# Kernel optimization log

Hardware: AMD Instinct MI355X
Metric: run time of the kernel (lower is better)

## Reference

```python
import jax, jax.numpy as jnp
import numpy as np

N_NODES = 100000
EMB_DIM = 128
HIDDEN = 128
N_EDGES = 1600000
N_LABEL = 200000


def _xavier(key, shape):
    fan_in, fan_out = shape[1], shape[0]
    lim = float(np.sqrt(6.0 / (fan_in + fan_out)))
    return jax.random.uniform(key, shape, jnp.float32, -lim, lim)


def setup_inputs() -> dict:
    key = jax.random.key(0)
    ks = jax.random.split(key, 8)
    n_id = jnp.arange(N_NODES, dtype=jnp.int64) if jax.config.jax_enable_x64 else jnp.arange(N_NODES, dtype=jnp.int32)
    edge_index = jax.random.randint(ks[0], (2, N_EDGES), 0, N_NODES)
    edge_label_index = jax.random.randint(ks[1], (2, N_LABEL), 0, N_NODES)
    emb_weight = _xavier(ks[2], (N_NODES, EMB_DIM))
    # layer 0: in=EMB_DIM -> HIDDEN ; layer 1: HIDDEN -> HIDDEN
    Wl0 = _xavier(ks[3], (HIDDEN, EMB_DIM))
    bl0 = jnp.zeros((HIDDEN,), jnp.float32)
    Wr0 = _xavier(ks[4], (HIDDEN, EMB_DIM))
    Wl1 = _xavier(ks[5], (HIDDEN, HIDDEN))
    bl1 = jnp.zeros((HIDDEN,), jnp.float32)
    Wr1 = _xavier(ks[6], (HIDDEN, HIDDEN))
    return {
        "n_id": n_id,
        "edge_index": edge_index,
        "edge_label_index": edge_label_index,
        "emb_weight": emb_weight,
        "Wl0": Wl0, "bl0": bl0, "Wr0": Wr0,
        "Wl1": Wl1, "bl1": bl1, "Wr1": Wr1,
    }


def _sage_conv(x, src, dst, Wl, bl, Wr, num_nodes):
    # PyG SAGEConv (aggr='mean'): out = lin_l(mean_{j in N(i)} x_j) + lin_r(x_i)
    agg = jax.ops.segment_sum(x[src], dst, num_segments=num_nodes)  # [N, D]
    deg = jax.ops.segment_sum(jnp.ones((src.shape[0],), x.dtype), dst, num_segments=num_nodes)
    mean = agg / jnp.maximum(deg, 1.0)[:, None]
    return mean @ Wl.T + bl + x @ Wr.T


def reference(n_id, edge_index, edge_label_index, emb_weight, Wl0, bl0, Wr0, Wl1, bl1, Wr1):
    src, dst = edge_index[0], edge_index[1]
    num_nodes = n_id.shape[0]
    x = emb_weight[n_id]                                  # [N, EMB_DIM]
    x = _sage_conv(x, src, dst, Wl0, bl0, Wr0, num_nodes)  # layer 0
    x = jax.nn.relu(x)                                     # relu between layers (dropout p=0, eval)
    z = _sage_conv(x, src, dst, Wl1, bl1, Wr1, num_nodes)  # layer 1 (no relu after last)
    s, d = edge_label_index[0], edge_label_index[1]
    return jnp.sum(z[s] * z[d], axis=-1)                   # [N_LABEL]
```

## Files before the change

### kernel.cpp

```cpp
#include <hip/hip_runtime.h>
#include <hip/hip_bf16.h>

typedef short bf16x8 __attribute__((ext_vector_type(8)));
typedef float f32x4 __attribute__((ext_vector_type(4)));
typedef float f32x2 __attribute__((ext_vector_type(2)));

#define BKT_SHIFT 9
#define BKT_RANGE 512
#define MAXBKT 256

__device__ __forceinline__ float bf2f(unsigned short u){
  union { unsigned int i; float f; } v; v.i = ((unsigned int)u)<<16; return v.f;
}
__device__ __forceinline__ unsigned short f2bf(float f){
  union { float f; unsigned int i; } v; v.f = f;
  unsigned int i = v.i;
  return (unsigned short)((i + 0x7fffu + ((i>>16)&1u)) >> 16);
}
__device__ __forceinline__ f32x2 up2(unsigned int v){
  union { unsigned int i; float f; } lo, hi;
  lo.i = v << 16; hi.i = v & 0xffff0000u;
  return (f32x2){lo.f, hi.f};
}

__global__ void k_bcount(const int* dst, int* gcount, int ne, int nbk){
  __shared__ int cnt[MAXBKT];
  int tid = threadIdx.x;
  if(tid < nbk) cnt[tid] = 0;
  __syncthreads();
  int base = blockIdx.x * 4096;
#pragma unroll
  for(int i=0;i<16;++i){
    int e = base + i*256 + tid;
    if(e < ne) atomicAdd(&cnt[dst[e] >> BKT_SHIFT], 1);
  }
  __syncthreads();
  if(tid < nbk && cnt[tid] > 0) atomicAdd(&gcount[tid], cnt[tid]);
}

__global__ void k_bscatter_prep(const int* src, const int* dst, const int* gcount,
                                int* gcur0, unsigned int* ebuf, int ne, int nbk, int nch,
                                const float* emb, const int* n_id, unsigned short* A0,
                                const float* Wl0, const float* Wr0, unsigned short* wc0,
                                const float* Wl1, const float* Wr1, unsigned short* wc1,
                                int n){
  int b = blockIdx.x;
  int tid = threadIdx.x;
  if(b >= nch){
    int pb = b - nch;
    if(pb < 256){
      const float* Wl = (pb < 128) ? Wl0 : Wl1;
      const float* Wr = (pb < 128) ? Wr0 : Wr1;
      unsigned short* wc = (pb < 128) ? wc0 : wc1;
      int i = (pb & 127)*256 + tid;
      int nn = i >> 8, k = i & 255;
      float v = (k<128) ? Wl[nn*128 + k] : Wr[nn*128 + k - 128];
      wc[i] = f2bf(v);
    } else {
      int gid = (pb-256)*256 + tid;
      int row = gid >> 5, c4 = (gid & 31) * 4;
      if(row >= n) return;
      float4 v = *(const float4*)&emb[(long)n_id[row]*128 + c4];
      ushort4 o;
      o.x = f2bf(v.x); o.y = f2bf(v.y); o.z = f2bf(v.z); o.w = f2bf(v.w);
      *(ushort4*)&A0[(long)row*256 + 128 + c4] = o;
    }
    return;
  }
  __shared__ int cnt[MAXBKT];
  __shared__ int runbase[MAXBKT];
  __shared__ int sg[MAXBKT];
  cnt[tid] = 0;
  sg[tid] = (tid < nbk) ? gcount[tid] : 0;
  __syncthreads();
  int base = b * 4096;
  int pk[16], bk[16], re[16];
#pragma unroll
  for(int i=0;i<16;++i){
    int e = base + i*256 + tid;
    if(e < ne){
      int d = dst[e];
      bk[i] = d >> BKT_SHIFT;
      pk[i] = (unsigned)src[e] | ((unsigned)(d & (BKT_RANGE-1)) << 17);
      re[i] = atomicAdd(&cnt[bk[i]], 1);
    } else bk[i] = -1;
  }
  int myv = sg[tid];
  __syncthreads();
  for(int off=1; off<256; off<<=1){
    int a = (tid>=off) ? sg[tid-off] : 0;
    __syncthreads();
    sg[tid] += a;
    __syncthreads();
  }
  if(tid < nbk)
    runbase[tid] = (sg[tid] - myv) + (cnt[tid] ? atomicAdd(&gcur0[tid], cnt[tid]) : 0);
  __syncthreads();
#pragma unroll
  for(int i=0;i<16;++i){
    if(bk[i] >= 0) ebuf[runbase[bk[i]] + re[i]] = pk[i];
  }
}

__global__ void k_bsort(const unsigned int* ebuf, const int* gcount,
                        int* csr, int* row_off, int n, int ne, int nbk){
  __shared__ int sg[MAXBKT];
  __shared__ int h[BKT_RANGE];
  __shared__ int cur[BKT_RANGE];
  __shared__ int sm[512];
  int t = threadIdx.x;
  int k = blockIdx.x;
  if(t < MAXBKT) sg[t] = (t < nbk) ? gcount[t] : 0;
  __syncthreads();
  for(int off=1; off<256; off<<=1){
    int a = (t>=off && t<256) ? sg[t-off] : 0;
    __syncthreads();
    if(t<256) sg[t] += a;
    __syncthreads();
  }
  int beg = sg[k] - gcount[k];
  int end = sg[k];
  int lo = k << BKT_SHIFT;
  h[t] = 0;
  __syncthreads();
  for(int e = beg + t; e < end; e += 512)
    atomicAdd(&h[ebuf[e] >> 17], 1);
  __syncthreads();
  int v = h[t];
  sm[t] = v;
  __syncthreads();
  for(int off=1; off<512; off<<=1){
    int a = (t>=off) ? sm[t-off] : 0;
    __syncthreads();
    sm[t] += a;
    __syncthreads();
  }
  int excl = beg + sm[t] - v;
  cur[t] = excl;
  if(lo + t < n) row_off[lo + t] = excl;
  if(k == nbk-1 && t == 0) row_off[n] = ne;
  __syncthreads();
  for(int e = beg + t; e < end; e += 512){
    unsigned int p = ebuf[e];
    int pos = atomicAdd(&cur[p >> 17], 1);
    csr[pos] = (int)(p & 0x1FFFFu);
  }
}

__global__ void k_agg(const unsigned short* X, unsigned short* Mout,
                      const int* row_off, const int* csr, int n){
  int w = __builtin_amdgcn_readfirstlane((int)((blockIdx.x*blockDim.x + threadIdx.x) >> 6));
  int lane = threadIdx.x & 63;
  if(w >= n) return;
  int beg = row_off[w], end = row_off[w+1];
  int deg = end - beg;
  f32x2 acc = {0.f, 0.f};
  const char* Xb = (const char*)X + 256;
  int e = beg;
  for(; e + 8 <= end; e += 8){
    unsigned int v0 = ((const unsigned int*)(Xb + (long)csr[e  ]*512))[lane];
    unsigned int v1 = ((const unsigned int*)(Xb + (long)csr[e+1]*512))[lane];
    unsigned int v2 = ((const unsigned int*)(Xb + (long)csr[e+2]*512))[lane];
    unsigned int v3 = ((const unsigned int*)(Xb + (long)csr[e+3]*512))[lane];
    unsigned int v4 = ((const unsigned int*)(Xb + (long)csr[e+4]*512))[lane];
    unsigned int v5 = ((const unsigned int*)(Xb + (long)csr[e+5]*512))[lane];
    unsigned int v6 = ((const unsigned int*)(Xb + (long)csr[e+6]*512))[lane];
    unsigned int v7 = ((const unsigned int*)(Xb + (long)csr[e+7]*512))[lane];
    acc += up2(v0); acc += up2(v1); acc += up2(v2); acc += up2(v3);
    acc += up2(v4); acc += up2(v5); acc += up2(v6); acc += up2(v7);
  }
  for(; e + 4 <= end; e += 4){
    unsigned int v0 = ((const unsigned int*)(Xb + (long)csr[e  ]*512))[lane];
    unsigned int v1 = ((const unsigned int*)(Xb + (long)csr[e+1]*512))[lane];
    unsigned int v2 = ((const unsigned int*)(Xb + (long)csr[e+2]*512))[lane];
    unsigned int v3 = ((const unsigned int*)(Xb + (long)csr[e+3]*512))[lane];
    acc += up2(v0); acc += up2(v1); acc += up2(v2); acc += up2(v3);
  }
  for(; e < end; ++e){
    unsigned int v = ((const unsigned int*)(Xb + (long)csr[e]*512))[lane];
    acc += up2(v);
  }
  float inv = (deg>0) ? 1.0f/(float)deg : 0.f;
  float a0 = acc[0]*inv, a1 = acc[1]*inv;
  unsigned int o = ((unsigned int)f2bf(a1) << 16) | (unsigned int)f2bf(a0);
  *(unsigned int*)((char*)Mout + (long)w*512 + lane*4) = o;
}

template<int RELU, int OUTSTRIDE, int OUTOFF>
__global__ __launch_bounds__(256,2) void k_gemm(const unsigned short* A,
                                                const unsigned short* wc,
                                                const float* bias,
                                                unsigned short* out, int nrows){
  __shared__ unsigned short Wl[32768];
  int tid = threadIdx.x;
  for(int it=0; it<16; ++it){
    int idx  = it*256 + tid;
    int byte = idx*16;
    int row  = byte >> 9;
    int swz  = byte ^ ((row & 7) << 4);
    *(uint4*)((char*)Wl + swz) = *(const uint4*)((const char*)wc + byte);
  }
  __syncthreads();

  int lane = tid & 63, wv = tid >> 6;
  float bs[8];
#pragma unroll
  for(int nf=0; nf<8; ++nf) bs[nf] = bias[nf*16 + (lane & 15)];

  for(int t=0; t<4; ++t){
    int rowA = blockIdx.x*256 + t*64 + wv*16 + (lane & 15);
    int rcl  = rowA < nrows ? rowA : nrows-1;
    const char* Ab = (const char*)(A + (long)rcl*256) + ((lane>>4)*16);
    bf16x8 a[8];
#pragma unroll
    for(int k=0;k<8;++k) a[k] = *(const bf16x8*)(Ab + k*64);

    f32x4 acc[8];
#pragma unroll
    for(int i=0;i<8;++i) acc[i] = (f32x4){0.f,0.f,0.f,0.f};

#pragma unroll
    for(int nf=0; nf<8; ++nf){
      int rw = nf*16 + (lane & 15);
#pragma unroll
      for(int k=0;k<8;++k){
        int byte = (rw*512 + k*64 + (lane>>4)*16) ^ ((rw & 7) << 4);
        bf16x8 b = *(const bf16x8*)((const char*)Wl + byte);
        acc[nf] = __builtin_amdgcn_mfma_f32_16x16x32_bf16(a[k], b, acc[nf], 0, 0, 0);
      }
    }

    int rbase = blockIdx.x*256 + t*64 + wv*16 + (lane>>4)*4;
#pragma unroll
    for(int nf=0; nf<8; ++nf){
      int col = nf*16 + (lane & 15);
#pragma unroll
      for(int r=0;r<4;++r){
        int row = rbase + r;
        if(row < nrows){
          float v = acc[nf][r] + bs[nf];
          if(RELU) v = v > 0.f ? v : 0.f;
          out[(long)row*OUTSTRIDE + OUTOFF + col] = f2bf(v);
        }
      }
    }
  }
}

__global__ void k_dot(const unsigned short* z, const int* s, const int* d,
                      float* out, int nl){
  int wv = (blockIdx.x*256 + threadIdx.x) >> 6;
  int lane = threadIdx.x & 63;
  int g = lane >> 4;
  int gl = lane & 15;
  int pi = wv*4 + g;
  float acc = 0.f;
  if(pi < nl){
    int si = s[pi], di = d[pi];
    bf16x8 va = *(const bf16x8*)&z[(long)si*128 + gl*8];
    bf16x8 vb = *(const bf16x8*)&z[(long)di*128 + gl*8];
#pragma unroll
    for(int i=0;i<8;++i)
      acc += bf2f((unsigned short)va[i]) * bf2f((unsigned short)vb[i]);
#pragma unroll
    for(int off=1; off<16; off<<=1)
      acc += __shfl_xor(acc, off, 16);
    if(gl==0) out[pi] = acc;
  }
}

extern "C" void kernel_launch(void* const* d_in, const int* in_sizes, int n_in,
                              void* d_out, int out_size, void* d_ws, size_t ws_size,
                              hipStream_t stream){
  const int N  = in_sizes[0];
  const int NE = in_sizes[1] / 2;
  const int NL = in_sizes[2] / 2;
  const int*   n_id = (const int*)d_in[0];
  const int*   src  = (const int*)d_in[1];
  const int*   dst  = src + NE;
  const int*   ls   = (const int*)d_in[2];
  const int*   ld   = ls + NL;
  const float* emb  = (const float*)d_in[3];
  const float* Wl0  = (const float*)d_in[4];
  const float* bl0  = (const float*)d_in[5];
  const float* Wr0  = (const float*)d_in[6];
  const float* Wl1  = (const float*)d_in[7];
  const float* bl1  = (const float*)d_in[8];
  const float* Wr1  = (const float*)d_in[9];
  float* out = (float*)d_out;

  char* ws = (char*)d_ws;
  size_t off = 0;
  auto alloc = [&](size_t bytes)->char*{
    char* p = ws + off;
    off = (off + bytes + 255) & ~(size_t)255;
    return p;
  };
  unsigned short* A0   = (unsigned short*)alloc((size_t)N*256*2);
  unsigned short* A1   = (unsigned short*)alloc((size_t)N*256*2);
  int* row_off         = (int*)alloc((size_t)(N+1)*4);
  int* csr             = (int*)alloc((size_t)NE*4);
  int* gcount          = (int*)alloc(MAXBKT*4*2);
  int* gcur0           = gcount + MAXBKT;
  unsigned short* wc0  = (unsigned short*)alloc(128*256*2);
  unsigned short* wc1  = (unsigned short*)alloc(128*256*2);
  unsigned int* ebuf   = (unsigned int*)A1;
  unsigned short* Z    = A0;

  const int NBK = (N + BKT_RANGE - 1) >> BKT_SHIFT;
  const int NCH = (NE + 4095) / 4096;

  hipMemsetAsync(gcount, 0, MAXBKT*4*2, stream);
  hipLaunchKernelGGL(k_bcount, dim3(NCH), dim3(256), 0, stream, dst, gcount, NE, NBK);
  hipLaunchKernelGGL(k_bscatter_prep, dim3(NCH + 256 + (N*32+255)/256), dim3(256), 0, stream,
                     src, dst, gcount, gcur0, ebuf, NE, NBK, NCH,
                     emb, n_id, A0, Wl0, Wr0, wc0, Wl1, Wr1, wc1, N);
  hipLaunchKernelGGL(k_bsort, dim3(NBK), dim3(512), 0, stream,
                     ebuf, gcount, csr, row_off, N, NE, NBK);
  hipLaunchKernelGGL(k_agg, dim3((N*64+255)/256), dim3(256), 0, stream, A0, A0, row_off, csr, N);
  hipLaunchKernelGGL((k_gemm<1,256,128>), dim3((N+255)/256), dim3(256), 0, stream, A0, wc0, bl0, A1, N);
  hipLaunchKernelGGL(k_agg, dim3((N*64+255)/256), dim3(256), 0, stream, A1, A1, row_off, csr, N);
  hipLaunchKernelGGL((k_gemm<0,128,0>), dim3((N+255)/256), dim3(256), 0, stream, A1, wc1, bl1, Z, N);
  hipLaunchKernelGGL(k_dot, dim3((NL+15)/16), dim3(256), 0, stream, Z, ls, ld, out, NL);
}
```

Baseline: 260.2 us.

## Fuse CSR bucket sort with layer-0 mean aggregation using smaller buckets

Buckets shrink from 512 to 128 destination nodes, and the bucket prefix scan moves into a separate single-block kernel, so the scatter and sort kernels no longer redo it per block. The per-bucket sort kernel now also performs the first layer's mean aggregation. It reads source indices from a shared-memory copy of the sorted bucket (with a global fallback when a bucket exceeds capacity), which removes one kernel launch and the CSR re-read. The cost is 782 blocks of 512 threads each doing only 128 nodes, so each wave handles 16 nodes serially, which may lower parallelism compared with the separate one-wave-per-node aggregation kernel.

```diff
diff --git a/kernel.cpp b/kernel.cpp
--- a/kernel.cpp
+++ b/kernel.cpp
@@ -5,9 +5,10 @@
 typedef float f32x4 __attribute__((ext_vector_type(4)));
 typedef float f32x2 __attribute__((ext_vector_type(2)));
 
-#define BKT_SHIFT 9
-#define BKT_RANGE 512
-#define MAXBKT 256
+#define BKT_SHIFT 7
+#define BKT_RANGE 128
+#define MAXBKT 1024
+#define CAP 4096
 
 __device__ __forceinline__ float bf2f(unsigned short u){
   union { unsigned int i; float f; } v; v.i = ((unsigned int)u)<<16; return v.f;
@@ -26,7 +27,7 @@
 __global__ void k_bcount(const int* dst, int* gcount, int ne, int nbk){
   __shared__ int cnt[MAXBKT];
   int tid = threadIdx.x;
-  if(tid < nbk) cnt[tid] = 0;
+  for(int i=tid; i<MAXBKT; i+=256) cnt[i] = 0;
   __syncthreads();
   int base = blockIdx.x * 4096;
 #pragma unroll
@@ -35,10 +36,26 @@
     if(e < ne) atomicAdd(&cnt[dst[e] >> BKT_SHIFT], 1);
   }
   __syncthreads();
-  if(tid < nbk && cnt[tid] > 0) atomicAdd(&gcount[tid], cnt[tid]);
-}
-
-__global__ void k_bscatter_prep(const int* src, const int* dst, const int* gcount,
+  for(int i=tid; i<nbk; i+=256) if(cnt[i]) atomicAdd(&gcount[i], cnt[i]);
+}
+
+__global__ void k_bscan(const int* gcount, int* gbase, int nbk, int ne){
+  __shared__ int sm[MAXBKT];
+  int t = threadIdx.x;
+  int v = (t<nbk) ? gcount[t] : 0;
+  sm[t] = v;
+  __syncthreads();
+  for(int off=1; off<MAXBKT; off<<=1){
+    int a = (t>=off) ? sm[t-off] : 0;
+    __syncthreads();
+    sm[t] += a;
+    __syncthreads();
+  }
+  if(t<nbk) gbase[t] = sm[t] - v;
+  if(t==nbk-1) gbase[nbk] = sm[t];
+}
+
+__global__ void k_bscatter_prep(const int* src, const int* dst, const int* gbase,
                                 int* gcur0, unsigned int* ebuf, int ne, int nbk, int nch,
                                 const float* emb, const int* n_id, unsigned short* A0,
                                 const float* Wl0, const float* Wr0, unsigned short* wc0,
@@ -69,9 +86,7 @@
   }
   __shared__ int cnt[MAXBKT];
   __shared__ int runbase[MAXBKT];
-  __shared__ int sg[MAXBKT];
-  cnt[tid] = 0;
-  sg[tid] = (tid < nbk) ? gcount[tid] : 0;
+  for(int i=tid; i<MAXBKT; i+=256) cnt[i] = 0;
   __syncthreads();
   int base = b * 4096;
   int pk[16], bk[16], re[16];
@@ -85,16 +100,9 @@
       re[i] = atomicAdd(&cnt[bk[i]], 1);
     } else bk[i] = -1;
   }
-  int myv = sg[tid];
-  __syncthreads();
-  for(int off=1; off<256; off<<=1){
-    int a = (tid>=off) ? sg[tid-off] : 0;
-    __syncthreads();
-    sg[tid] += a;
-    __syncthreads();
-  }
-  if(tid < nbk)
-    runbase[tid] = (sg[tid] - myv) + (cnt[tid] ? atomicAdd(&gcur0[tid], cnt[tid]) : 0);
+  __syncthreads();
+  for(int i=tid; i<nbk; i+=256)
+    runbase[i] = gbase[i] + (cnt[i] ? atomicAdd(&gcur0[i], cnt[i]) : 0);
   __syncthreads();
 #pragma unroll
   for(int i=0;i<16;++i){
@@ -102,48 +110,104 @@
   }
 }
 
-__global__ void k_bsort(const unsigned int* ebuf, const int* gcount,
-                        int* csr, int* row_off, int n, int ne, int nbk){
-  __shared__ int sg[MAXBKT];
+__global__ __launch_bounds__(512) void k_aggsort(const unsigned int* ebuf, const int* gbase,
+                                                 const unsigned short* X, unsigned short* Mout,
+                                                 int* csr, int* row_off, int n, int ne, int nbk){
   __shared__ int h[BKT_RANGE];
+  __shared__ int ends[BKT_RANGE];
   __shared__ int cur[BKT_RANGE];
-  __shared__ int sm[512];
-  int t = threadIdx.x;
-  int k = blockIdx.x;
-  if(t < MAXBKT) sg[t] = (t < nbk) ? gcount[t] : 0;
-  __syncthreads();
-  for(int off=1; off<256; off<<=1){
-    int a = (t>=off && t<256) ? sg[t-off] : 0;
+  __shared__ int eb[CAP];
+  int t = threadIdx.x, k = blockIdx.x;
+  int beg = gbase[k], end = gbase[k+1];
+  int cnt = end - beg;
+  bool lok = (cnt <= CAP);
+  if(t < BKT_RANGE) h[t] = 0;
+  __syncthreads();
+  for(int e=t; e<cnt; e+=512) atomicAdd(&h[ebuf[beg+e] >> 17], 1);
+  __syncthreads();
+  int v0 = (t < BKT_RANGE) ? h[t] : 0;
+  for(int off=1; off<BKT_RANGE; off<<=1){
+    int a = (t>=off && t<BKT_RANGE) ? h[t-off] : 0;
     __syncthreads();
-    if(t<256) sg[t] += a;
+    if(t<BKT_RANGE) h[t] += a;
     __syncthreads();
   }
-  int beg = sg[k] - gcount[k];
-  int end = sg[k];
-  int lo = k << BKT_SHIFT;
-  h[t] = 0;
-  __syncthreads();
-  for(int e = beg + t; e < end; e += 512)
-    atomicAdd(&h[ebuf[e] >> 17], 1);
-  __syncthreads();
-  int v = h[t];
-  sm[t] = v;
-  __syncthreads();
-  for(int off=1; off<512; off<<=1){
-    int a = (t>=off) ? sm[t-off] : 0;
-    __syncthreads();
-    sm[t] += a;
-    __syncthreads();
-  }
-  int excl = beg + sm[t] - v;
-  cur[t] = excl;
-  if(lo + t < n) row_off[lo + t] = excl;
-  if(k == nbk-1 && t == 0) row_off[n] = ne;
-  __syncthreads();
-  for(int e = beg + t; e < end; e += 512){
-    unsigned int p = ebuf[e];
+  if(t < BKT_RANGE){
+    ends[t] = h[t];
+    cur[t]  = h[t] - v0;
+    int node = (k<<BKT_SHIFT) + t;
+    if(node < n) row_off[node] = beg + h[t] - v0;
+  }
+  if(k==nbk-1 && t==0) row_off[n] = ne;
+  __syncthreads();
+  for(int e=t; e<cnt; e+=512){
+    unsigned int p = ebuf[beg+e];
     int pos = atomicAdd(&cur[p >> 17], 1);
-    csr[pos] = (int)(p & 0x1FFFFu);
+    int s = (int)(p & 0x1FFFFu);
+    if(lok) eb[pos] = s;
+    csr[beg + pos] = s;
+  }
+  __syncthreads();
+  int wv = t >> 6, lane = t & 63;
+  const char* Xb = (const char*)X + 256;
+  const int* gsrc = csr + beg;
+  for(int i = wv*16; i < wv*16+16; ++i){
+    int node = (k<<BKT_SHIFT) + i;
+    if(node >= n) continue;
+    int lbeg = i ? ends[i-1] : 0;
+    int lend = ends[i];
+    int deg = lend - lbeg;
+    f32x2 acc = {0.f, 0.f};
+    if(lok){
+      int e = lbeg;
+      for(; e+8 <= lend; e += 8){
+        int s0=eb[e],s1=eb[e+1],s2=eb[e+2],s3=eb[e+3],s4=eb[e+4],s5=eb[e+5],s6=eb[e+6],s7=eb[e+7];
+        unsigned int v0 = ((const unsigned int*)(Xb + (long)s0*512))[lane];
+        unsigned int v1 = ((const unsigned int*)(Xb + (long)s1*512))[lane];
+        unsigned int v2 = ((const unsigned int*)(Xb + (long)s2*512))[lane];
+        unsigned int v3 = ((const unsigned int*)(Xb + (long)s3*512))[lane];
+        unsigned int v4 = ((const unsigned int*)(Xb + (long)s4*512))[lane];
+        unsigned int v5 = ((const unsigned int*)(Xb + (long)s5*512))[lane];
+        unsigned int v6 = ((const unsigned int*)(Xb + (long)s6*512))[lane];
+        unsigned int v7 = ((const unsigned int*)(Xb + (long)s7*512))[lane];
+        acc += up2(v0); acc += up2(v1); acc += up2(v2); acc += up2(v3);
+        acc += up2(v4); acc += up2(v5); acc += up2(v6); acc += up2(v7);
+      }
+      for(; e+4 <= lend; e += 4){
+        int s0=eb[e],s1=eb[e+1],s2=eb[e+2],s3=eb[e+3];
+        unsigned int v0 = ((const unsigned int*)(Xb + (long)s0*512))[lane];
+        unsigned int v1 = ((const unsigned int*)(Xb + (long)s1*512))[lane];
+        unsigned int v2 = ((const unsigned int*)(Xb + (long)s2*512))[lane];
+        unsigned int v3 = ((const unsigned int*)(Xb + (long)s3*512))[lane];
+        acc += up2(v0); acc += up2(v1); acc += up2(v2); acc += up2(v3);
+      }
+      for(; e < lend; ++e){
+        unsigned int v = ((const unsigned int*)(Xb + (long)eb[e]*512))[lane];
+        acc += up2(v);
+      }
+    } else {
+      int e = lbeg;
+      for(; e+8 <= lend; e += 8){
+        int s0=gsrc[e],s1=gsrc[e+1],s2=gsrc[e+2],s3=gsrc[e+3],s4=gsrc[e+4],s5=gsrc[e+5],s6=gsrc[e+6],s7=gsrc[e+7];
+        unsigned int v0 = ((const unsigned int*)(Xb + (long)s0*512))[lane];
+        unsigned int v1 = ((const unsigned int*)(Xb + (long)s1*512))[lane];
+        unsigned int v2 = ((const unsigned int*)(Xb + (long)s2*512))[lane];
+        unsigned int v3 = ((const unsigned int*)(Xb + (long)s3*512))[lane];
+        unsigned int v4 = ((const unsigned int*)(Xb + (long)s4*512))[lane];
+        unsigned int v5 = ((const unsigned int*)(Xb + (long)s5*512))[lane];
+        unsigned int v6 = ((const unsigned int*)(Xb + (long)s6*512))[lane];
+        unsigned int v7 = ((const unsigned int*)(Xb + (long)s7*512))[lane];
+        acc += up2(v0); acc += up2(v1); acc += up2(v2); acc += up2(v3);
+        acc += up2(v4); acc += up2(v5); acc += up2(v6); acc += up2(v7);
+      }
+      for(; e < lend; ++e){
+        unsigned int v = ((const unsigned int*)(Xb + (long)gsrc[e]*512))[lane];
+        acc += up2(v);
+      }
+    }
+    float inv = (deg>0) ? 1.0f/(float)deg : 0.f;
+    unsigned int o = ((unsigned int)f2bf(acc[1]*inv) << 16) | (unsigned int)f2bf(acc[0]*inv);
+    *(unsigned int*)((char*)Mout + (long)node*512 + lane*4) = o;
   }
 }
 
@@ -300,8 +364,9 @@
   unsigned short* A1   = (unsigned short*)alloc((size_t)N*256*2);
   int* row_off         = (int*)alloc((size_t)(N+1)*4);
   int* csr             = (int*)alloc((size_t)NE*4);
-  int* gcount          = (int*)alloc(MAXBKT*4*2);
+  int* gcount          = (int*)alloc(MAXBKT*4*3 + 4);
   int* gcur0           = gcount + MAXBKT;
+  int* gbase           = gcount + MAXBKT*2;
   unsigned short* wc0  = (unsigned short*)alloc(128*256*2);
   unsigned short* wc1  = (unsigned short*)alloc(128*256*2);
   unsigned int* ebuf   = (unsigned int*)A1;
@@ -312,12 +377,12 @@
 
   hipMemsetAsync(gcount, 0, MAXBKT*4*2, stream);
   hipLaunchKernelGGL(k_bcount, dim3(NCH), dim3(256), 0, stream, dst, gcount, NE, NBK);
+  hipLaunchKernelGGL(k_bscan, dim3(1), dim3(MAXBKT), 0, stream, gcount, gbase, NBK, NE);
   hipLaunchKernelGGL(k_bscatter_prep, dim3(NCH + 256 + (N*32+255)/256), dim3(256), 0, stream,
-                     src, dst, gcount, gcur0, ebuf, NE, NBK, NCH,
+                     src, dst, gbase, gcur0, ebuf, NE, NBK, NCH,
                      emb, n_id, A0, Wl0, Wr0, wc0, Wl1, Wr1, wc1, N);
-  hipLaunchKernelGGL(k_bsort, dim3(NBK), dim3(512), 0, stream,
-                     ebuf, gcount, csr, row_off, N, NE, NBK);
-  hipLaunchKernelGGL(k_agg, dim3((N*64+255)/256), dim3(256), 0, stream, A0, A0, row_off, csr, N);
+  hipLaunchKernelGGL(k_aggsort, dim3(NBK), dim3(512), 0, stream,
+                     ebuf, gbase, A0, A0, csr, row_off, N, NE, NBK);
   hipLaunchKernelGGL((k_gemm<1,256,128>), dim3((N+255)/256), dim3(256), 0, stream, A0, wc0, bl0, A1, N);
   hipLaunchKernelGGL(k_agg, dim3((N*64+255)/256), dim3(256), 0, stream, A1, A1, row_off, csr, N);
   hipLaunchKernelGGL((k_gemm<0,128,0>), dim3((N+255)/256), dim3(256), 0, stream, A1, wc1, bl1, Z, N);
```

Result: slower. 267.1 us (+2.6%).

## Split aggregation into feature slices with edge-parallel lanes and wave reduction

Applied to the files above, without the earlier changes.

Restructures the mean-aggregation kernel so each block handles one 32-byte feature slice (of 8) for a run of nodes. Lanes within a wave are spread across 8 edges at a time instead of 64 lanes covering one full row, and a shuffle reduction combines the partial sums. The aim is to raise memory-level parallelism and to make concurrently running blocks that share a slice reuse the same L2 lines. Loads and stores are marked nontemporal. The cost is much less bytes per gather (32B segments), plus extra shuffle and masking work; low-degree nodes waste lanes.

```diff
diff --git a/kernel.cpp b/kernel.cpp
--- a/kernel.cpp
+++ b/kernel.cpp
@@ -8,6 +8,7 @@
 #define BKT_SHIFT 9
 #define BKT_RANGE 512
 #define MAXBKT 256
+#define NPW 8
 
 __device__ __forceinline__ float bf2f(unsigned short u){
   union { unsigned int i; float f; } v; v.i = ((unsigned int)u)<<16; return v.f;
@@ -149,41 +150,48 @@
 
 __global__ void k_agg(const unsigned short* X, unsigned short* Mout,
                       const int* row_off, const int* csr, int n){
-  int w = __builtin_amdgcn_readfirstlane((int)((blockIdx.x*blockDim.x + threadIdx.x) >> 6));
+  int s = blockIdx.x & 7;
+  int chunk = blockIdx.x >> 3;
+  int wv = threadIdx.x >> 6;
   int lane = threadIdx.x & 63;
-  if(w >= n) return;
-  int beg = row_off[w], end = row_off[w+1];
-  int deg = end - beg;
-  f32x2 acc = {0.f, 0.f};
-  const char* Xb = (const char*)X + 256;
-  int e = beg;
-  for(; e + 8 <= end; e += 8){
-    unsigned int v0 = ((const unsigned int*)(Xb + (long)csr[e  ]*512))[lane];
-    unsigned int v1 = ((const unsigned int*)(Xb + (long)csr[e+1]*512))[lane];
-    unsigned int v2 = ((const unsigned int*)(Xb + (long)csr[e+2]*512))[lane];
-    unsigned int v3 = ((const unsigned int*)(Xb + (long)csr[e+3]*512))[lane];
-    unsigned int v4 = ((const unsigned int*)(Xb + (long)csr[e+4]*512))[lane];
-    unsigned int v5 = ((const unsigned int*)(Xb + (long)csr[e+5]*512))[lane];
-    unsigned int v6 = ((const unsigned int*)(Xb + (long)csr[e+6]*512))[lane];
-    unsigned int v7 = ((const unsigned int*)(Xb + (long)csr[e+7]*512))[lane];
-    acc += up2(v0); acc += up2(v1); acc += up2(v2); acc += up2(v3);
-    acc += up2(v4); acc += up2(v5); acc += up2(v6); acc += up2(v7);
-  }
-  for(; e + 4 <= end; e += 4){
-    unsigned int v0 = ((const unsigned int*)(Xb + (long)csr[e  ]*512))[lane];
-    unsigned int v1 = ((const unsigned int*)(Xb + (long)csr[e+1]*512))[lane];
-    unsigned int v2 = ((const unsigned int*)(Xb + (long)csr[e+2]*512))[lane];
-    unsigned int v3 = ((const unsigned int*)(Xb + (long)csr[e+3]*512))[lane];
-    acc += up2(v0); acc += up2(v1); acc += up2(v2); acc += up2(v3);
-  }
-  for(; e < end; ++e){
-    unsigned int v = ((const unsigned int*)(Xb + (long)csr[e]*512))[lane];
-    acc += up2(v);
-  }
-  float inv = (deg>0) ? 1.0f/(float)deg : 0.f;
-  float a0 = acc[0]*inv, a1 = acc[1]*inv;
-  unsigned int o = ((unsigned int)f2bf(a1) << 16) | (unsigned int)f2bf(a0);
-  *(unsigned int*)((char*)Mout + (long)w*512 + lane*4) = o;
+  int eg = lane >> 3;
+  int bl = lane & 7;
+  int n0 = __builtin_amdgcn_readfirstlane((chunk*4 + wv) * NPW);
+  const char* Xs = (const char*)X + 256 + s*32 + bl*4;
+  char* Ms = (char*)Mout + s*32 + bl*4;
+#pragma unroll 1
+  for(int i=0; i<NPW; ++i){
+    int w = n0 + i;
+    if(w >= n) return;
+    int beg = row_off[w], end = row_off[w+1];
+    int deg = end - beg;
+    int c1 = deg - 1;
+    f32x2 acc = {0.f, 0.f};
+#pragma unroll 1
+    for(int base=0; base<deg; base+=16){
+      int e0 = base + eg, e1 = base + 8 + eg;
+      int i0 = e0 > c1 ? c1 : e0;
+      int i1 = e1 > c1 ? c1 : e1;
+      int x0 = __builtin_nontemporal_load(&csr[beg + i0]);
+      int x1 = __builtin_nontemporal_load(&csr[beg + i1]);
+      unsigned int v0 = *(const unsigned int*)(Xs + (long)x0*512);
+      unsigned int v1 = *(const unsigned int*)(Xs + (long)x1*512);
+      if(e0 > c1) v0 = 0;
+      if(e1 > c1) v1 = 0;
+      acc += up2(v0);
+      acc += up2(v1);
+    }
+#pragma unroll
+    for(int off=8; off<64; off<<=1){
+      acc[0] += __shfl_xor(acc[0], off);
+      acc[1] += __shfl_xor(acc[1], off);
+    }
+    if(eg == 0){
+      float inv = (deg>0) ? 1.0f/(float)deg : 0.f;
+      unsigned int o = ((unsigned)f2bf(acc[1]*inv) << 16) | f2bf(acc[0]*inv);
+      __builtin_nontemporal_store(o, (unsigned int*)(Ms + (long)w*512));
+    }
+  }
 }
 
 template<int RELU, int OUTSTRIDE, int OUTOFF>
@@ -309,6 +317,7 @@
 
   const int NBK = (N + BKT_RANGE - 1) >> BKT_SHIFT;
   const int NCH = (NE + 4095) / 4096;
+  const int AGG_BLOCKS = 8 * ((N + 4*NPW - 1) / (4*NPW));
 
   hipMemsetAsync(gcount, 0, MAXBKT*4*2, stream);
   hipLaunchKernelGGL(k_bcount, dim3(NCH), dim3(256), 0, stream, dst, gcount, NE, NBK);
@@ -317,9 +326,9 @@
                      emb, n_id, A0, Wl0, Wr0, wc0, Wl1, Wr1, wc1, N);
   hipLaunchKernelGGL(k_bsort, dim3(NBK), dim3(512), 0, stream,
                      ebuf, gcount, csr, row_off, N, NE, NBK);
-  hipLaunchKernelGGL(k_agg, dim3((N*64+255)/256), dim3(256), 0, stream, A0, A0, row_off, csr, N);
+  hipLaunchKernelGGL(k_agg, dim3(AGG_BLOCKS), dim3(256), 0, stream, A0, A0, row_off, csr, N);
   hipLaunchKernelGGL((k_gemm<1,256,128>), dim3((N+255)/256), dim3(256), 0, stream, A0, wc0, bl0, A1, N);
-  hipLaunchKernelGGL(k_agg, dim3((N*64+255)/256), dim3(256), 0, stream, A1, A1, row_off, csr, N);
+  hipLaunchKernelGGL(k_agg, dim3(AGG_BLOCKS), dim3(256), 0, stream, A1, A1, row_off, csr, N);
   hipLaunchKernelGGL((k_gemm<0,128,0>), dim3((N+255)/256), dim3(256), 0, stream, A1, wc1, bl1, Z, N);
   hipLaunchKernelGGL(k_dot, dim3((NL+15)/16), dim3(256), 0, stream, Z, ls, ld, out, NL);
 }
```

Result: slower. 673.8 us (+158.9%).
